# Kernel optimization log

Hardware: AMD Instinct MI355X
Metric: run time of the kernel (lower is better)

The kernel has to match this reference:

```python
import jax, jax.numpy as jnp
import numpy as np

N_NODES = 100000
N_EDGES = 3200000
IN_CH, H1, H2, N_CLS = 128, 32, 20, 10
EPS = 1e-12  # F.normalize eps


def _glorot(key, shape):
    fan_in = shape[0]
    return jax.random.normal(key, shape, dtype=jnp.float32) / np.sqrt(fan_in)


def setup_inputs() -> dict:
    key = jax.random.key(0)
    ks = jax.random.split(key, 9)
    x = jax.random.normal(ks[0], (N_NODES, IN_CH), dtype=jnp.float32)
    edge_index = jax.random.randint(ks[1], (2, N_EDGES), 0, N_NODES, dtype=jnp.int64)
    return {
        "x": x,
        "edge_index": edge_index,
        "W1_l": _glorot(ks[2], (IN_CH, H1)),
        "b1_l": jnp.zeros((H1,), jnp.float32),
        "W1_r": _glorot(ks[3], (IN_CH, H1)),
        "W2_l": _glorot(ks[4], (H1, H2)),
        "b2_l": jnp.zeros((H2,), jnp.float32),
        "W2_r": _glorot(ks[5], (H1, H2)),
        "W_out": _glorot(ks[6], (H2, N_CLS)),
        "b_out": jnp.zeros((N_CLS,), jnp.float32),
    }


def _sage_conv(x, src, dst, W_l, b_l, W_r, n_nodes):
    # mean-aggregate neighbor features: scatter x[src] into dst buckets
    agg = jax.ops.segment_sum(x[src], dst, num_segments=n_nodes)  # [N, F]
    deg = jax.ops.segment_sum(jnp.ones((src.shape[0], 1), x.dtype), dst,
                              num_segments=n_nodes)
    agg = agg / jnp.maximum(deg, 1.0)
    out = agg @ W_l + b_l + x @ W_r  # lin_l(agg) + lin_r(x), lin_r has no bias
    # normalize=True -> L2 normalize per node
    nrm = jnp.maximum(jnp.linalg.norm(out, axis=-1, keepdims=True), EPS)
    return out / nrm


def reference(x, edge_index, W1_l, b1_l, W1_r, W2_l, b2_l, W2_r, W_out, b_out):
    src, dst = edge_index[0], edge_index[1]
    n = x.shape[0]
    h = _sage_conv(x, src, dst, W1_l, b1_l, W1_r, n)
    h = jax.nn.relu(h)
    # dropout(p=0.5) is identity in eval mode
    h = _sage_conv(h, src, dst, W2_l, b2_l, W2_r, n)
    logits = h @ W_out + b_out
    return jax.nn.softmax(logits, axis=1)
```

## Files before the change

### kernel.cpp

```cpp
#include <hip/hip_runtime.h>
#include <hip/hip_fp16.h>
#include <math.h>


#define BSHIFT 7
#define BS_NODES 128
#define PART_TILE 8192

__device__ __forceinline__ unsigned pk(float a, float b) {
    __half2 h = __floats2half2_rn(a, b);
    return *reinterpret_cast<unsigned*>(&h);
}

__global__ __launch_bounds__(256) void k_binit(
    int* __restrict__ bcursor, int nb, int capb)
{
    int i = blockIdx.x * 256 + threadIdx.x;
    if (i < nb) bcursor[i] = i * capb;
}

__global__ __launch_bounds__(256) void k_part(
    const int* __restrict__ src, const int* __restrict__ dst,
    int* __restrict__ bcursor, int* __restrict__ pairs,
    int n_edges, int nb)
{
    __shared__ int cnt[1024];
    __shared__ int bbase_l[1024];
    int tid = threadIdx.x;
    int ebeg = blockIdx.x * PART_TILE;
    int eend = ebeg + PART_TILE; if (eend > n_edges) eend = n_edges;
    for (int i = tid; i < nb; i += 256) cnt[i] = 0;
    __syncthreads();
    for (int e = ebeg + tid; e < eend; e += 256)
        atomicAdd(&cnt[dst[e] >> BSHIFT], 1);
    __syncthreads();
    for (int i = tid; i < nb; i += 256) {
        int c = cnt[i];
        if (c > 0) bbase_l[i] = atomicAdd(&bcursor[i], c);
    }
    __syncthreads();
    for (int e = ebeg + tid; e < eend; e += 256) {
        int d = dst[e];
        int b = d >> BSHIFT;
        int slot = atomicSub(&cnt[b], 1) - 1;
        pairs[(size_t)bbase_l[b] + slot] = (src[e] << BSHIFT) | (d & (BS_NODES - 1));
    }
}

__global__ __launch_bounds__(1024) void k_bscan(
    const int* __restrict__ bcursor, int* __restrict__ bbase,
    int* __restrict__ row_ptr, int nb, int capb, int n_nodes)
{
    __shared__ int sc[1024];
    int t = threadIdx.x;
    int c = (t < nb) ? (bcursor[t] - t * capb) : 0;
    sc[t] = c;
    __syncthreads();
    for (int off = 1; off < 1024; off <<= 1) {
        int v = (t >= off) ? sc[t - off] : 0;
        __syncthreads();
        sc[t] += v;
        __syncthreads();
    }
    if (t < nb) bbase[t] = sc[t] - c;
    if (t == 1023) row_ptr[n_nodes] = sc[t];
}

__global__ __launch_bounds__(256) void k_bfill(
    const int* __restrict__ pairs, const int* __restrict__ bcursor,
    const int* __restrict__ bbase, int* __restrict__ row_ptr,
    int* __restrict__ eid, int capb, int n_nodes)
{
    __shared__ int cnt128[BS_NODES];
    __shared__ int sc[BS_NODES];
    __shared__ int cur[BS_NODES];
    int b = blockIdx.x;
    int t = threadIdx.x;
    int lo = b * BS_NODES;
    size_t pbeg = (size_t)b * capb;
    int cntE = bcursor[b] - b * capb;
    int base = bbase[b];
    if (t < BS_NODES) cnt128[t] = 0;
    __syncthreads();
    for (int i = t; i < cntE; i += 256)
        atomicAdd(&cnt128[pairs[pbeg + i] & (BS_NODES - 1)], 1);
    __syncthreads();
    int myc = 0;
    if (t < BS_NODES) { myc = cnt128[t]; sc[t] = myc; }
    __syncthreads();
    for (int off = 1; off < BS_NODES; off <<= 1) {
        int v = (t >= off && t < BS_NODES) ? sc[t - off] : 0;
        __syncthreads();
        if (t < BS_NODES) sc[t] += v;
        __syncthreads();
    }
    if (t < BS_NODES) {
        int excl = sc[t] - myc;
        cur[t] = excl;
        if (lo + t < n_nodes) row_ptr[lo + t] = base + excl;
    }
    __syncthreads();
    for (int i = t; i < cntE; i += 256) {
        int p = pairs[pbeg + i];
        int pos = atomicAdd(&cur[p & (BS_NODES - 1)], 1);
        eid[(size_t)base + pos] = p >> BSHIFT;
    }
}

__global__ __launch_bounds__(256) void k_lin1(
    const float* __restrict__ x, const float* __restrict__ W1l,
    const float* __restrict__ b1, const float* __restrict__ W1r,
    __half* __restrict__ y1, __half* __restrict__ r1, int n_nodes)
{
    __shared__ unsigned lds[256 * 64];
    int tid = threadIdx.x;
    int base = blockIdx.x * 256;
    const float4* x4 = reinterpret_cast<const float4*>(x);
#pragma unroll
    for (int it = 0; it < 32; ++it) {
        int f = it * 256 + tid;
        int row = f >> 5, c4 = f & 31;
        int node = base + row;
        float4 v = make_float4(0.f, 0.f, 0.f, 0.f);
        if (node < n_nodes) v = x4[(size_t)node * 32 + c4];
        int kk = c4 * 2;
        lds[row * 64 + ((kk + row) & 63)]     = pk(v.x, v.y);
        lds[row * 64 + ((kk + 1 + row) & 63)] = pk(v.z, v.w);
    }
    __syncthreads();
    int node = base + tid;
    float accL[32], accR[32];
#pragma unroll
    for (int j = 0; j < 32; ++j) { accL[j] = 0.f; accR[j] = 0.f; }
    const unsigned* rb = &lds[tid * 64];
    for (int kk = 0; kk < 64; ++kk) {
        unsigned u = rb[(kk + tid) & 63];
        __half2 hh = *reinterpret_cast<__half2*>(&u);
        float2 f = __half22float2(hh);
        const float* wl = W1l + kk * 64;
        const float* wr = W1r + kk * 64;
#pragma unroll
        for (int j = 0; j < 32; ++j) {
            float a = accL[j];
            a = fmaf(f.x, wl[j],      a);
            a = fmaf(f.y, wl[32 + j], a);
            accL[j] = a;
            float c = accR[j];
            c = fmaf(f.x, wr[j],      c);
            c = fmaf(f.y, wr[32 + j], c);
            accR[j] = c;
        }
    }
    if (node < n_nodes) {
        unsigned o[16];
#pragma unroll
        for (int q = 0; q < 16; ++q) o[q] = pk(accL[2*q], accL[2*q+1]);
        uint4* yo = reinterpret_cast<uint4*>(y1 + (size_t)node * 32);
#pragma unroll
        for (int q = 0; q < 4; ++q)
            yo[q] = make_uint4(o[4*q], o[4*q+1], o[4*q+2], o[4*q+3]);
#pragma unroll
        for (int q = 0; q < 16; ++q)
            o[q] = pk(accR[2*q] + b1[2*q], accR[2*q+1] + b1[2*q+1]);
        uint4* ro = reinterpret_cast<uint4*>(r1 + (size_t)node * 32);
#pragma unroll
        for (int q = 0; q < 4; ++q)
            ro[q] = make_uint4(o[4*q], o[4*q+1], o[4*q+2], o[4*q+3]);
    }
}

__device__ __forceinline__ float gather_sum(
    const int* __restrict__ eid, const __half* __restrict__ tab,
    int beg, int end, int ch)
{
    float s0 = 0.f, s1 = 0.f, s2 = 0.f, s3 = 0.f;
    float s4 = 0.f, s5 = 0.f, s6 = 0.f, s7 = 0.f;
    int i = beg;
    for (; i + 8 <= end; i += 8) {
        int e0 = eid[i];
        int e1 = eid[i + 1];
        int e2 = eid[i + 2];
        int e3 = eid[i + 3];
        int e4 = eid[i + 4];
        int e5 = eid[i + 5];
        int e6 = eid[i + 6];
        int e7 = eid[i + 7];
        s0 += __half2float(tab[(size_t)e0 * 32 + ch]);
        s1 += __half2float(tab[(size_t)e1 * 32 + ch]);
        s2 += __half2float(tab[(size_t)e2 * 32 + ch]);
        s3 += __half2float(tab[(size_t)e3 * 32 + ch]);
        s4 += __half2float(tab[(size_t)e4 * 32 + ch]);
        s5 += __half2float(tab[(size_t)e5 * 32 + ch]);
        s6 += __half2float(tab[(size_t)e6 * 32 + ch]);
        s7 += __half2float(tab[(size_t)e7 * 32 + ch]);
    }
    for (; i + 4 <= end; i += 4) {
        int e0 = eid[i];
        int e1 = eid[i + 1];
        int e2 = eid[i + 2];
        int e3 = eid[i + 3];
        s0 += __half2float(tab[(size_t)e0 * 32 + ch]);
        s1 += __half2float(tab[(size_t)e1 * 32 + ch]);
        s2 += __half2float(tab[(size_t)e2 * 32 + ch]);
        s3 += __half2float(tab[(size_t)e3 * 32 + ch]);
    }
    for (; i < end; ++i) {
        int e = eid[i];
        s0 += __half2float(tab[(size_t)e * 32 + ch]);
    }
    return ((s0 + s1) + (s2 + s3)) + ((s4 + s5) + (s6 + s7));
}

__global__ __launch_bounds__(256) void k_agg1(
    const int* __restrict__ row_ptr, const int* __restrict__ eid,
    const __half* __restrict__ y1, const __half* __restrict__ r1,
    const float* __restrict__ W2l, const float* __restrict__ W2r,
    const float* __restrict__ b2,
    __half* __restrict__ z2, __half* __restrict__ r2, int n_nodes)
{
    int t = blockIdx.x * 256 + threadIdx.x;
    int n = t >> 5;
    int ch = t & 31;
    if (n >= n_nodes) return;
    int beg = row_ptr[n], end = row_ptr[n + 1];
    float sum = gather_sum(eid, y1, beg, end, ch);
    float inv = 1.0f / fmaxf((float)(end - beg), 1.0f);
    float v = fmaf(sum, inv, __half2float(r1[(size_t)n * 32 + ch]));
    float ss = v * v;
#pragma unroll
    for (int off = 16; off >= 1; off >>= 1) ss += __shfl_xor(ss, off, 32);
    float h = fmaxf(v / fmaxf(sqrtf(ss), 1e-12f), 0.f);
    float accl = 0.f, accr = 0.f;
#pragma unroll 4
    for (int ii = 0; ii < 32; ++ii) {
        float hv = __shfl(h, ii, 32);
        if (ch < 20) {
            accl = fmaf(hv, W2l[ii * 20 + ch], accl);
            accr = fmaf(hv, W2r[ii * 20 + ch], accr);
        }
    }
    z2[(size_t)n * 32 + ch] = __float2half(ch < 20 ? accl : 0.f);
    r2[(size_t)n * 32 + ch] = __float2half(ch < 20 ? accr + b2[ch] : 0.f);
}

__global__ __launch_bounds__(256) void k_agg2(
    const int* __restrict__ row_ptr, const int* __restrict__ eid,
    const __half* __restrict__ z2, const __half* __restrict__ r2,
    const float* __restrict__ Wout, const float* __restrict__ bout,
    float* __restrict__ out, int n_nodes)
{
    int t = blockIdx.x * 256 + threadIdx.x;
    int n = t >> 5;
    int ch = t & 31;
    if (n >= n_nodes) return;
    int beg = row_ptr[n], end = row_ptr[n + 1];
    bool act = ch < 20;
    float sum = gather_sum(eid, z2, beg, end, ch);
    float inv = 1.0f / fmaxf((float)(end - beg), 1.0f);
    float v = act ? fmaf(sum, inv, __half2float(r2[(size_t)n * 32 + ch])) : 0.f;
    float ss = v * v;
#pragma unroll
    for (int off = 16; off >= 1; off >>= 1) ss += __shfl_xor(ss, off, 32);
    float o = v / fmaxf(sqrtf(ss), 1e-12f);
    float acc = (ch < 10) ? bout[ch] : 0.f;
#pragma unroll 4
    for (int ii = 0; ii < 20; ++ii) {
        float ov = __shfl(o, ii, 32);
        if (ch < 10) acc = fmaf(ov, Wout[ii * 10 + ch], acc);
    }
    float lm = (ch < 10) ? acc : -1e30f;
    float m = lm;
#pragma unroll
    for (int off = 8; off >= 1; off >>= 1) m = fmaxf(m, __shfl_xor(m, off, 16));
    float ex = (ch < 10) ? expf(acc - m) : 0.f;
    float s2r = ex;
#pragma unroll
    for (int off = 8; off >= 1; off >>= 1) s2r += __shfl_xor(s2r, off, 16);
    if (ch < 10) out[(size_t)n * 10 + ch] = ex / s2r;
}

extern "C" void kernel_launch(void* const* d_in, const int* in_sizes, int n_in,
                              void* d_out, int out_size, void* d_ws, size_t ws_size,
                              hipStream_t stream)
{
    const float* x    = (const float*)d_in[0];
    const int*   ei   = (const int*)d_in[1];
    const float* W1l  = (const float*)d_in[2];
    const float* b1   = (const float*)d_in[3];
    const float* W1r  = (const float*)d_in[4];
    const float* W2l  = (const float*)d_in[5];
    const float* b2   = (const float*)d_in[6];
    const float* W2r  = (const float*)d_in[7];
    const float* Wout = (const float*)d_in[8];
    const float* bout = (const float*)d_in[9];
    float* out = (float*)d_out;

    int n_nodes = in_sizes[0] / 128;
    int n_edges = in_sizes[1] / 2;
    const int* src = ei;
    const int* dst = ei + n_edges;

    int nb = (n_nodes + BS_NODES - 1) / BS_NODES;
    double mean = (double)n_edges / nb;
    int capb = (int)(mean + 8.0 * sqrt(mean) + 64.0);
    capb = (capb + 63) & ~63;

    int* bcursor = (int*)d_ws;
    int* bbase   = bcursor + ((nb + 2 + 3) & ~3);
    int* row_ptr = bbase + ((nb + 3) & ~3);
    int* eid     = row_ptr + (((n_nodes + 1) + 3) & ~3);
    int* pairs   = eid + (((size_t)n_edges + 3) & ~(size_t)3);

    __half* y1 = (__half*)pairs;
    __half* r1 = y1 + (size_t)n_nodes * 32;
    __half* z2 = r1 + (size_t)n_nodes * 32;
    __half* r2 = z2 + (size_t)n_nodes * 32;

    int nb_part = (n_edges + PART_TILE - 1) / PART_TILE;
    int nb_node = (n_nodes + 255) / 256;
    int nb_grp  = ((n_nodes * 32) + 255) / 256;

    k_binit<<<(nb + 255) / 256, 256, 0, stream>>>(bcursor, nb, capb);
    k_part<<<nb_part, 256, 0, stream>>>(src, dst, bcursor, pairs, n_edges, nb);
    k_bscan<<<1, 1024, 0, stream>>>(bcursor, bbase, row_ptr, nb, capb, n_nodes);
    k_bfill<<<nb, 256, 0, stream>>>(pairs, bcursor, bbase, row_ptr, eid, capb, n_nodes);
    k_lin1<<<nb_node, 256, 0, stream>>>(x, W1l, b1, W1r, y1, r1, n_nodes);
    k_agg1<<<nb_grp, 256, 0, stream>>>(row_ptr, eid, y1, r1, W2l, W2r, b2, z2, r2, n_nodes);
    k_agg2<<<nb_grp, 256, 0, stream>>>(row_ptr, eid, z2, r2, Wout, bout, out, n_nodes);
}
```

Measured before the change: 322.8 us.

## Drop global bucket scan, fuse bucket fill with first linear layer, use padded CSR

Removes the single-block bucket scan and the init kernel. Edges now stay in fixed-capacity padded bucket slots, and each node gets an explicit (begin,end) int2 range instead of a prefix-summed row pointer. The bucket-fill work and the first dense layer run as two block roles inside one launch, so the lin1 GEMM overlaps the CSR build and two launches go away. It also adds nontemporal loads for the second gather. In exchange, eid and pairs need padded buffers, which enlarges the workspace and makes eid accesses sparser.

Measured after the change: 342.3 us. 1.06x slower.

```diff
diff --git a/kernel.cpp b/kernel.cpp
--- a/kernel.cpp
+++ b/kernel.cpp
@@ -12,17 +12,15 @@
     return *reinterpret_cast<unsigned*>(&h);
 }
 
-__global__ __launch_bounds__(256) void k_binit(
-    int* __restrict__ bcursor, int nb, int capb)
-{
-    int i = blockIdx.x * 256 + threadIdx.x;
-    if (i < nb) bcursor[i] = i * capb;
+__device__ __forceinline__ float h2f_bits(unsigned short u) {
+    __half_raw hr; hr.x = u;
+    return __half2float(__half(hr));
 }
 
 __global__ __launch_bounds__(256) void k_part(
     const int* __restrict__ src, const int* __restrict__ dst,
     int* __restrict__ bcursor, int* __restrict__ pairs,
-    int n_edges, int nb)
+    int n_edges, int nb, int capb)
 {
     __shared__ int cnt[1024];
     __shared__ int bbase_l[1024];
@@ -43,138 +41,123 @@
         int d = dst[e];
         int b = d >> BSHIFT;
         int slot = atomicSub(&cnt[b], 1) - 1;
-        pairs[(size_t)bbase_l[b] + slot] = (src[e] << BSHIFT) | (d & (BS_NODES - 1));
-    }
-}
-
-__global__ __launch_bounds__(1024) void k_bscan(
-    const int* __restrict__ bcursor, int* __restrict__ bbase,
-    int* __restrict__ row_ptr, int nb, int capb, int n_nodes)
-{
-    __shared__ int sc[1024];
-    int t = threadIdx.x;
-    int c = (t < nb) ? (bcursor[t] - t * capb) : 0;
-    sc[t] = c;
-    __syncthreads();
-    for (int off = 1; off < 1024; off <<= 1) {
-        int v = (t >= off) ? sc[t - off] : 0;
-        __syncthreads();
-        sc[t] += v;
-        __syncthreads();
-    }
-    if (t < nb) bbase[t] = sc[t] - c;
-    if (t == 1023) row_ptr[n_nodes] = sc[t];
-}
-
-__global__ __launch_bounds__(256) void k_bfill(
+        pairs[(size_t)b * capb + bbase_l[b] + slot] =
+            (src[e] << BSHIFT) | (d & (BS_NODES - 1));
+    }
+}
+
+__global__ __launch_bounds__(256) void k_prep(
     const int* __restrict__ pairs, const int* __restrict__ bcursor,
-    const int* __restrict__ bbase, int* __restrict__ row_ptr,
-    int* __restrict__ eid, int capb, int n_nodes)
-{
-    __shared__ int cnt128[BS_NODES];
-    __shared__ int sc[BS_NODES];
-    __shared__ int cur[BS_NODES];
-    int b = blockIdx.x;
-    int t = threadIdx.x;
-    int lo = b * BS_NODES;
-    size_t pbeg = (size_t)b * capb;
-    int cntE = bcursor[b] - b * capb;
-    int base = bbase[b];
-    if (t < BS_NODES) cnt128[t] = 0;
-    __syncthreads();
-    for (int i = t; i < cntE; i += 256)
-        atomicAdd(&cnt128[pairs[pbeg + i] & (BS_NODES - 1)], 1);
-    __syncthreads();
-    int myc = 0;
-    if (t < BS_NODES) { myc = cnt128[t]; sc[t] = myc; }
-    __syncthreads();
-    for (int off = 1; off < BS_NODES; off <<= 1) {
-        int v = (t >= off && t < BS_NODES) ? sc[t - off] : 0;
-        __syncthreads();
-        if (t < BS_NODES) sc[t] += v;
-        __syncthreads();
-    }
-    if (t < BS_NODES) {
-        int excl = sc[t] - myc;
-        cur[t] = excl;
-        if (lo + t < n_nodes) row_ptr[lo + t] = base + excl;
-    }
-    __syncthreads();
-    for (int i = t; i < cntE; i += 256) {
-        int p = pairs[pbeg + i];
-        int pos = atomicAdd(&cur[p & (BS_NODES - 1)], 1);
-        eid[(size_t)base + pos] = p >> BSHIFT;
-    }
-}
-
-__global__ __launch_bounds__(256) void k_lin1(
+    int2* __restrict__ row2, int* __restrict__ eid,
     const float* __restrict__ x, const float* __restrict__ W1l,
     const float* __restrict__ b1, const float* __restrict__ W1r,
-    __half* __restrict__ y1, __half* __restrict__ r1, int n_nodes)
+    __half* __restrict__ y1, __half* __restrict__ r1,
+    int capb, int n_nodes, int nb)
 {
     __shared__ unsigned lds[256 * 64];
     int tid = threadIdx.x;
-    int base = blockIdx.x * 256;
-    const float4* x4 = reinterpret_cast<const float4*>(x);
-#pragma unroll
-    for (int it = 0; it < 32; ++it) {
-        int f = it * 256 + tid;
-        int row = f >> 5, c4 = f & 31;
-        int node = base + row;
-        float4 v = make_float4(0.f, 0.f, 0.f, 0.f);
-        if (node < n_nodes) v = x4[(size_t)node * 32 + c4];
-        int kk = c4 * 2;
-        lds[row * 64 + ((kk + row) & 63)]     = pk(v.x, v.y);
-        lds[row * 64 + ((kk + 1 + row) & 63)] = pk(v.z, v.w);
-    }
-    __syncthreads();
-    int node = base + tid;
-    float accL[32], accR[32];
-#pragma unroll
-    for (int j = 0; j < 32; ++j) { accL[j] = 0.f; accR[j] = 0.f; }
-    const unsigned* rb = &lds[tid * 64];
-    for (int kk = 0; kk < 64; ++kk) {
-        unsigned u = rb[(kk + tid) & 63];
-        __half2 hh = *reinterpret_cast<__half2*>(&u);
-        float2 f = __half22float2(hh);
-        const float* wl = W1l + kk * 64;
-        const float* wr = W1r + kk * 64;
-#pragma unroll
-        for (int j = 0; j < 32; ++j) {
-            float a = accL[j];
-            a = fmaf(f.x, wl[j],      a);
-            a = fmaf(f.y, wl[32 + j], a);
-            accL[j] = a;
-            float c = accR[j];
-            c = fmaf(f.x, wr[j],      c);
-            c = fmaf(f.y, wr[32 + j], c);
-            accR[j] = c;
-        }
-    }
-    if (node < n_nodes) {
-        unsigned o[16];
-#pragma unroll
-        for (int q = 0; q < 16; ++q) o[q] = pk(accL[2*q], accL[2*q+1]);
-        uint4* yo = reinterpret_cast<uint4*>(y1 + (size_t)node * 32);
-#pragma unroll
-        for (int q = 0; q < 4; ++q)
-            yo[q] = make_uint4(o[4*q], o[4*q+1], o[4*q+2], o[4*q+3]);
-#pragma unroll
-        for (int q = 0; q < 16; ++q)
-            o[q] = pk(accR[2*q] + b1[2*q], accR[2*q+1] + b1[2*q+1]);
-        uint4* ro = reinterpret_cast<uint4*>(r1 + (size_t)node * 32);
-#pragma unroll
-        for (int q = 0; q < 4; ++q)
-            ro[q] = make_uint4(o[4*q], o[4*q+1], o[4*q+2], o[4*q+3]);
-    }
-}
-
+    if ((int)blockIdx.x < nb) {
+        int* cnt128 = (int*)lds;
+        int* sc     = cnt128 + BS_NODES;
+        int* cur    = sc + BS_NODES;
+        int b = blockIdx.x;
+        int lo = b * BS_NODES;
+        size_t base = (size_t)b * capb;
+        int cntE = bcursor[b];
+        if (tid < BS_NODES) cnt128[tid] = 0;
+        __syncthreads();
+        for (int i = tid; i < cntE; i += 256)
+            atomicAdd(&cnt128[pairs[base + i] & (BS_NODES - 1)], 1);
+        __syncthreads();
+        int myc = 0;
+        if (tid < BS_NODES) { myc = cnt128[tid]; sc[tid] = myc; }
+        __syncthreads();
+        for (int off = 1; off < BS_NODES; off <<= 1) {
+            int v = (tid >= off && tid < BS_NODES) ? sc[tid - off] : 0;
+            __syncthreads();
+            if (tid < BS_NODES) sc[tid] += v;
+            __syncthreads();
+        }
+        if (tid < BS_NODES) {
+            int excl = sc[tid] - myc;
+            cur[tid] = excl;
+            if (lo + tid < n_nodes)
+                row2[lo + tid] = make_int2((int)base + excl,
+                                           (int)base + excl + myc);
+        }
+        __syncthreads();
+        for (int i = tid; i < cntE; i += 256) {
+            int p = pairs[base + i];
+            int pos = atomicAdd(&cur[p & (BS_NODES - 1)], 1);
+            eid[base + pos] = p >> BSHIFT;
+        }
+    } else {
+        int nodebase = (blockIdx.x - nb) * 256;
+        const float4* x4 = reinterpret_cast<const float4*>(x);
+#pragma unroll
+        for (int it = 0; it < 32; ++it) {
+            int f = it * 256 + tid;
+            int row = f >> 5, c4 = f & 31;
+            int node = nodebase + row;
+            float4 v = make_float4(0.f, 0.f, 0.f, 0.f);
+            if (node < n_nodes) v = x4[(size_t)node * 32 + c4];
+            int kk = c4 * 2;
+            lds[row * 64 + ((kk + row) & 63)]     = pk(v.x, v.y);
+            lds[row * 64 + ((kk + 1 + row) & 63)] = pk(v.z, v.w);
+        }
+        __syncthreads();
+        int node = nodebase + tid;
+        float accL[32], accR[32];
+#pragma unroll
+        for (int j = 0; j < 32; ++j) { accL[j] = 0.f; accR[j] = 0.f; }
+        const unsigned* rb = &lds[tid * 64];
+        for (int kk = 0; kk < 64; ++kk) {
+            unsigned u = rb[(kk + tid) & 63];
+            __half2 hh = *reinterpret_cast<__half2*>(&u);
+            float2 f = __half22float2(hh);
+            const float* wl = W1l + kk * 64;
+            const float* wr = W1r + kk * 64;
+#pragma unroll
+            for (int j = 0; j < 32; ++j) {
+                float a = accL[j];
+                a = fmaf(f.x, wl[j],      a);
+                a = fmaf(f.y, wl[32 + j], a);
+                accL[j] = a;
+                float c = accR[j];
+                c = fmaf(f.x, wr[j],      c);
+                c = fmaf(f.y, wr[32 + j], c);
+                accR[j] = c;
+            }
+        }
+        if (node < n_nodes) {
+            unsigned o[16];
+#pragma unroll
+            for (int q = 0; q < 16; ++q) o[q] = pk(accL[2*q], accL[2*q+1]);
+            uint4* yo = reinterpret_cast<uint4*>(y1 + (size_t)node * 32);
+#pragma unroll
+            for (int q = 0; q < 4; ++q)
+                yo[q] = make_uint4(o[4*q], o[4*q+1], o[4*q+2], o[4*q+3]);
+#pragma unroll
+            for (int q = 0; q < 16; ++q)
+                o[q] = pk(accR[2*q] + b1[2*q], accR[2*q+1] + b1[2*q+1]);
+            uint4* ro = reinterpret_cast<uint4*>(r1 + (size_t)node * 32);
+#pragma unroll
+            for (int q = 0; q < 4; ++q)
+                ro[q] = make_uint4(o[4*q], o[4*q+1], o[4*q+2], o[4*q+3]);
+        }
+    }
+}
+
+template <bool NT>
 __device__ __forceinline__ float gather_sum(
     const int* __restrict__ eid, const __half* __restrict__ tab,
     int beg, int end, int ch)
 {
+    const unsigned short* tb = reinterpret_cast<const unsigned short*>(tab);
     float s0 = 0.f, s1 = 0.f, s2 = 0.f, s3 = 0.f;
     float s4 = 0.f, s5 = 0.f, s6 = 0.f, s7 = 0.f;
+#define LD(e) h2f_bits(NT ? __builtin_nontemporal_load(&tb[(size_t)(e) * 32 + ch]) \
+                          : tb[(size_t)(e) * 32 + ch])
     int i = beg;
     for (; i + 8 <= end; i += 8) {
         int e0 = eid[i];
@@ -185,34 +168,35 @@
         int e5 = eid[i + 5];
         int e6 = eid[i + 6];
         int e7 = eid[i + 7];
-        s0 += __half2float(tab[(size_t)e0 * 32 + ch]);
-        s1 += __half2float(tab[(size_t)e1 * 32 + ch]);
-        s2 += __half2float(tab[(size_t)e2 * 32 + ch]);
-        s3 += __half2float(tab[(size_t)e3 * 32 + ch]);
-        s4 += __half2float(tab[(size_t)e4 * 32 + ch]);
-        s5 += __half2float(tab[(size_t)e5 * 32 + ch]);
-        s6 += __half2float(tab[(size_t)e6 * 32 + ch]);
-        s7 += __half2float(tab[(size_t)e7 * 32 + ch]);
+        s0 += LD(e0);
+        s1 += LD(e1);
+        s2 += LD(e2);
+        s3 += LD(e3);
+        s4 += LD(e4);
+        s5 += LD(e5);
+        s6 += LD(e6);
+        s7 += LD(e7);
     }
     for (; i + 4 <= end; i += 4) {
         int e0 = eid[i];
         int e1 = eid[i + 1];
         int e2 = eid[i + 2];
         int e3 = eid[i + 3];
-        s0 += __half2float(tab[(size_t)e0 * 32 + ch]);
-        s1 += __half2float(tab[(size_t)e1 * 32 + ch]);
-        s2 += __half2float(tab[(size_t)e2 * 32 + ch]);
-        s3 += __half2float(tab[(size_t)e3 * 32 + ch]);
+        s0 += LD(e0);
+        s1 += LD(e1);
+        s2 += LD(e2);
+        s3 += LD(e3);
     }
     for (; i < end; ++i) {
         int e = eid[i];
-        s0 += __half2float(tab[(size_t)e * 32 + ch]);
-    }
+        s0 += LD(e);
+    }
+#undef LD
     return ((s0 + s1) + (s2 + s3)) + ((s4 + s5) + (s6 + s7));
 }
 
 __global__ __launch_bounds__(256) void k_agg1(
-    const int* __restrict__ row_ptr, const int* __restrict__ eid,
+    const int2* __restrict__ row2, const int* __restrict__ eid,
     const __half* __restrict__ y1, const __half* __restrict__ r1,
     const float* __restrict__ W2l, const float* __restrict__ W2r,
     const float* __restrict__ b2,
@@ -222,9 +206,9 @@
     int n = t >> 5;
     int ch = t & 31;
     if (n >= n_nodes) return;
-    int beg = row_ptr[n], end = row_ptr[n + 1];
-    float sum = gather_sum(eid, y1, beg, end, ch);
-    float inv = 1.0f / fmaxf((float)(end - beg), 1.0f);
+    int2 be = row2[n];
+    float sum = gather_sum<false>(eid, y1, be.x, be.y, ch);
+    float inv = 1.0f / fmaxf((float)(be.y - be.x), 1.0f);
     float v = fmaf(sum, inv, __half2float(r1[(size_t)n * 32 + ch]));
     float ss = v * v;
 #pragma unroll
@@ -244,7 +228,7 @@
 }
 
 __global__ __launch_bounds__(256) void k_agg2(
-    const int* __restrict__ row_ptr, const int* __restrict__ eid,
+    const int2* __restrict__ row2, const int* __restrict__ eid,
     const __half* __restrict__ z2, const __half* __restrict__ r2,
     const float* __restrict__ Wout, const float* __restrict__ bout,
     float* __restrict__ out, int n_nodes)
@@ -253,10 +237,10 @@
     int n = t >> 5;
     int ch = t & 31;
     if (n >= n_nodes) return;
-    int beg = row_ptr[n], end = row_ptr[n + 1];
+    int2 be = row2[n];
     bool act = ch < 20;
-    float sum = gather_sum(eid, z2, beg, end, ch);
-    float inv = 1.0f / fmaxf((float)(end - beg), 1.0f);
+    float sum = gather_sum<true>(eid, z2, be.x, be.y, ch);
+    float inv = 1.0f / fmaxf((float)(be.y - be.x), 1.0f);
     float v = act ? fmaf(sum, inv, __half2float(r2[(size_t)n * 32 + ch])) : 0.f;
     float ss = v * v;
 #pragma unroll
@@ -305,26 +289,25 @@
     int capb = (int)(mean + 8.0 * sqrt(mean) + 64.0);
     capb = (capb + 63) & ~63;
 
-    int* bcursor = (int*)d_ws;
-    int* bbase   = bcursor + ((nb + 2 + 3) & ~3);
-    int* row_ptr = bbase + ((nb + 3) & ~3);
-    int* eid     = row_ptr + (((n_nodes + 1) + 3) & ~3);
-    int* pairs   = eid + (((size_t)n_edges + 3) & ~(size_t)3);
-
-    __half* y1 = (__half*)pairs;
+    int*  bcursor = (int*)d_ws;
+    int2* row2    = (int2*)((char*)d_ws + (((size_t)nb * 4 + 15) & ~(size_t)15));
+    int*  pairs   = (int*)(row2 + n_nodes);
+    size_t npairs = ((size_t)nb * capb + 3) & ~(size_t)3;
+    int*  eid     = pairs + npairs;
+    __half* y1 = (__half*)(eid + npairs);
     __half* r1 = y1 + (size_t)n_nodes * 32;
-    __half* z2 = r1 + (size_t)n_nodes * 32;
+    __half* z2 = (__half*)pairs;
     __half* r2 = z2 + (size_t)n_nodes * 32;
 
     int nb_part = (n_edges + PART_TILE - 1) / PART_TILE;
-    int nb_node = (n_nodes + 255) / 256;
+    int nbl     = (n_nodes + 255) / 256;
     int nb_grp  = ((n_nodes * 32) + 255) / 256;
 
-    k_binit<<<(nb + 255) / 256, 256, 0, stream>>>(bcursor, nb, capb);
-    k_part<<<nb_part, 256, 0, stream>>>(src, dst, bcursor, pairs, n_edges, nb);
-    k_bscan<<<1, 1024, 0, stream>>>(bcursor, bbase, row_ptr, nb, capb, n_nodes);
-    k_bfill<<<nb, 256, 0, stream>>>(pairs, bcursor, bbase, row_ptr, eid, capb, n_nodes);
-    k_lin1<<<nb_node, 256, 0, stream>>>(x, W1l, b1, W1r, y1, r1, n_nodes);
-    k_agg1<<<nb_grp, 256, 0, stream>>>(row_ptr, eid, y1, r1, W2l, W2r, b2, z2, r2, n_nodes);
-    k_agg2<<<nb_grp, 256, 0, stream>>>(row_ptr, eid, z2, r2, Wout, bout, out, n_nodes);
-}
+    (void)hipMemsetAsync(bcursor, 0, (size_t)nb * sizeof(int), stream);
+    k_part<<<nb_part, 256, 0, stream>>>(src, dst, bcursor, pairs, n_edges, nb, capb);
+    k_prep<<<nb + nbl, 256, 0, stream>>>(pairs, bcursor, row2, eid,
+                                         x, W1l, b1, W1r, y1, r1,
+                                         capb, n_nodes, nb);
+    k_agg1<<<nb_grp, 256, 0, stream>>>(row2, eid, y1, r1, W2l, W2r, b2, z2, r2, n_nodes);
+    k_agg2<<<nb_grp, 256, 0, stream>>>(row2, eid, z2, r2, Wout, bout, out, n_nodes);
+}
```
